# Kernel optimization log

Hardware: AMD Instinct MI355X
Metric: run time of the kernel (lower is better)

Reference implementation:

```python
import jax, jax.numpy as jnp
import numpy as np

N, E = 50000, 800000
IN_DIM, OUT_DIM, REL_DIM = 128, 64, 32
NEG_SLOPE = 0.01  # torch F.leaky_relu default


def setup_inputs() -> dict:
    key = jax.random.key(0)
    ks = jax.random.split(key, 12)
    return {
        "h": jax.random.normal(ks[0], (N, IN_DIM), jnp.float32),
        "relation": jax.random.normal(ks[1], (E, REL_DIM), jnp.float32),
        "score": jax.random.normal(ks[2], (E, 1), jnp.float32),
        "timestamp": jax.random.normal(ks[3], (E, 1), jnp.float32),
        "src": jax.random.randint(ks[4], (E,), 0, N, jnp.int32),
        "dst": jax.random.randint(ks[5], (E,), 0, N, jnp.int32),
        "W_n": jax.random.normal(ks[6], (IN_DIM, OUT_DIM), jnp.float32) / np.sqrt(IN_DIM),
        "W_r": jax.random.normal(ks[7], (REL_DIM, OUT_DIM), jnp.float32) / np.sqrt(REL_DIM),
        "W_s": jax.random.normal(ks[8], (1, OUT_DIM), jnp.float32),
        "W_t": jax.random.normal(ks[9], (1, OUT_DIM), jnp.float32),
        "a": jax.random.normal(ks[10], (5 * OUT_DIM,), jnp.float32) / np.sqrt(5 * OUT_DIM),
    }


def reference(h, relation, score, timestamp, src, dst, W_n, W_r, W_s, W_t, a):
    D = W_n.shape[1]
    z = h @ W_n                     # (N, D)
    er = relation @ W_r             # (E, D)
    es = score @ W_s                # (E, D)
    et = timestamp @ W_t            # (E, D)
    z_src = z[src]                  # (E, D) gather
    z_dst = z[dst]                  # (E, D) gather
    # attn_fc on concat([z_src, z_dst, er, es, et]) == sum of slice dot-products
    a1, a2, a3, a4, a5 = (a[0:D], a[D:2*D], a[2*D:3*D], a[3*D:4*D], a[4*D:5*D])
    logit = z_src @ a1 + z_dst @ a2 + er @ a3 + es @ a4 + et @ a5  # (E,)
    logit = jnp.where(logit >= 0, logit, NEG_SLOPE * logit)        # leaky_relu
    # segment softmax over edges grouped by dst node
    n = z.shape[0]
    seg_max = jax.ops.segment_max(logit, dst, num_segments=n)     # (N,)
    ex = jnp.exp(logit - seg_max[dst])                             # (E,)
    seg_sum = jax.ops.segment_sum(ex, dst, num_segments=n)        # (N,)
    alpha = ex / seg_sum[dst]                                      # (E,)
    # weighted scatter-sum of source features to dst nodes
    h_out = jax.ops.segment_sum(alpha[:, None] * z_src, dst, num_segments=n)  # (N, D)
    return h_out
```

## Files before the change

### kernel.cpp

```cpp
#include <hip/hip_runtime.h>

#define IN_DIM 128
#define OUT_DIM 64
#define REL_DIM 32
#define NEG_SLOPE 0.01f
#define CAP 64
#define EPB 1024
#define BCAP 1536
#define HSTRIDE 800

__global__ __launch_bounds__(256) void k_node(const float* __restrict__ h,
                                              const float* __restrict__ W_n,
                                              const float* __restrict__ a,
                                              float* __restrict__ z,
                                              float* __restrict__ s1,
                                              float* __restrict__ s2, int n) {
    __shared__ float hs[IN_DIM * 65];
    __shared__ float s1p[4][64], s2p[4][64];
    int base = blockIdx.x * 64;

    for (int i = threadIdx.x; i < 64 * 32; i += 256) {
        int r = i >> 5;
        int c4 = i & 31;
        float4 v = make_float4(0.f, 0.f, 0.f, 0.f);
        if (base + r < n) v = ((const float4*)(h + (size_t)(base + r) * IN_DIM))[c4];
        int k0 = c4 * 4;
        hs[(k0 + 0) * 65 + r] = v.x;
        hs[(k0 + 1) * 65 + r] = v.y;
        hs[(k0 + 2) * 65 + r] = v.z;
        hs[(k0 + 3) * 65 + r] = v.w;
    }
    __syncthreads();

    int lane = threadIdx.x & 63;
    int w = __builtin_amdgcn_readfirstlane(threadIdx.x >> 6);
    int c0 = w * 16;
    int row = base + lane;

    float acc[16];
    #pragma unroll
    for (int j = 0; j < 16; ++j) acc[j] = 0.f;

    const float* __restrict__ Wslice = W_n + c0;
    #pragma unroll 4
    for (int k = 0; k < IN_DIM; ++k) {
        float hv = hs[k * 65 + lane];
        const float* __restrict__ Wr = Wslice + k * OUT_DIM;
        #pragma unroll
        for (int j = 0; j < 16; ++j) acc[j] = fmaf(hv, Wr[j], acc[j]);
    }

    float p1 = 0.f, p2 = 0.f;
    #pragma unroll
    for (int j = 0; j < 16; ++j) {
        p1 = fmaf(acc[j], a[c0 + j], p1);
        p2 = fmaf(acc[j], a[OUT_DIM + c0 + j], p2);
    }
    s1p[w][lane] = p1;
    s2p[w][lane] = p2;

    if (row < n) {
        float4* zp = (float4*)(z + (size_t)row * OUT_DIM + c0);
        zp[0] = make_float4(acc[0], acc[1], acc[2], acc[3]);
        zp[1] = make_float4(acc[4], acc[5], acc[6], acc[7]);
        zp[2] = make_float4(acc[8], acc[9], acc[10], acc[11]);
        zp[3] = make_float4(acc[12], acc[13], acc[14], acc[15]);
    }
    __syncthreads();
    if (threadIdx.x < 64 && base + (int)threadIdx.x < n) {
        int l = threadIdx.x;
        s1[base + l] = s1p[0][l] + s1p[1][l] + s1p[2][l] + s1p[3][l];
        s2[base + l] = s2p[0][l] + s2p[1][l] + s2p[2][l] + s2p[3][l];
    }
}

__global__ __launch_bounds__(256) void k_hist(const int* __restrict__ dst,
                                              int* __restrict__ hist, int E, int nbkt) {
    __shared__ int lh[HSTRIDE];
    int t = threadIdx.x;
    for (int i = t; i < nbkt; i += 256) lh[i] = 0;
    __syncthreads();
    int e0 = blockIdx.x * EPB;
    #pragma unroll
    for (int i = 0; i < EPB / 256; ++i) {
        int e = e0 + i * 256 + t;
        if (e < E) atomicAdd(&lh[dst[e] >> 6], 1);
    }
    __syncthreads();
    for (int b = t; b < nbkt; b += 256)
        hist[(size_t)blockIdx.x * HSTRIDE + b] = lh[b];
}

__global__ __launch_bounds__(1024) void k_scan(int* __restrict__ hist,
                                               int* __restrict__ bcnt, int nblk) {
    __shared__ int tmp[1024];
    int b = blockIdx.x;
    int t = threadIdx.x;
    int v = (t < nblk) ? hist[(size_t)t * HSTRIDE + b] : 0;
    tmp[t] = v;
    __syncthreads();
    #pragma unroll
    for (int o = 1; o < 1024; o <<= 1) {
        int x = (t >= o) ? tmp[t - o] : 0;
        __syncthreads();
        tmp[t] += x;
        __syncthreads();
    }
    if (t < nblk) hist[(size_t)t * HSTRIDE + b] = tmp[t] - v;
    if (t == 0) bcnt[b] = tmp[1023];
}

__global__ __launch_bounds__(256) void k_scatter(const float* __restrict__ rel,
                                                 const float* __restrict__ score,
                                                 const float* __restrict__ ts,
                                                 const int* __restrict__ src,
                                                 const int* __restrict__ dst,
                                                 const float* __restrict__ s1,
                                                 const float* __restrict__ s2,
                                                 const float* __restrict__ W_r,
                                                 const float* __restrict__ W_s,
                                                 const float* __restrict__ W_t,
                                                 const float* __restrict__ a,
                                                 const int* __restrict__ hist,
                                                 int2* __restrict__ rec2,
                                                 int E, int nbkt) {
    __shared__ __align__(16) float cw[36];
    __shared__ int   lsrc[EPB], ldst[EPB];
    __shared__ float lsc[EPB],  lts[EPB];
    __shared__ int   lrank[HSTRIDE], lbase[HSTRIDE];
    int t = threadIdx.x;
    int e0 = blockIdx.x * EPB;

    if (t < REL_DIM) {
        const float* a3 = a + 2 * OUT_DIM;
        float acc = 0.f;
        #pragma unroll
        for (int d2 = 0; d2 < OUT_DIM; ++d2)
            acc = fmaf(W_r[t * OUT_DIM + d2], a3[d2], acc);
        cw[t] = acc;
    } else if (t == 32) {
        float acc = 0.f;
        for (int d2 = 0; d2 < OUT_DIM; ++d2) acc = fmaf(W_s[d2], a[3 * OUT_DIM + d2], acc);
        cw[32] = acc;
    } else if (t == 33) {
        float acc = 0.f;
        for (int d2 = 0; d2 < OUT_DIM; ++d2) acc = fmaf(W_t[d2], a[4 * OUT_DIM + d2], acc);
        cw[33] = acc;
    }
    for (int i = t; i < nbkt; i += 256) {
        lrank[i] = 0;
        lbase[i] = hist[(size_t)blockIdx.x * HSTRIDE + i];
    }
    #pragma unroll
    for (int i = 0; i < EPB / 256; ++i) {
        int le = i * 256 + t;
        int e = e0 + le;
        if (e < E) {
            lsrc[le] = src[e];
            ldst[le] = dst[e];
            lsc[le]  = score[e];
            lts[le]  = ts[e];
        }
    }
    __syncthreads();

    int g = t >> 3;
    int sub = t & 7;
    #pragma unroll 1
    for (int it = 0; it < EPB / 32; ++it) {
        int le = it * 32 + g;
        int e = e0 + le;
        if (e < E) {
            float4 w4 = ((const float4*)cw)[sub];
            float4 v = ((const float4*)rel)[(size_t)e * 8 + sub];
            float dot = v.x * w4.x + v.y * w4.y + v.z * w4.z + v.w * w4.w;
            dot += __shfl_xor(dot, 1, 8);
            dot += __shfl_xor(dot, 2, 8);
            dot += __shfl_xor(dot, 4, 8);
            if (sub == 0) {
                int s = lsrc[le], d = ldst[le];
                float lg = dot + s1[s] + s2[d] + lsc[le] * cw[32] + lts[le] * cw[33];
                lg = (lg >= 0.f) ? lg : NEG_SLOPE * lg;
                int b = d >> 6;
                int lr = atomicAdd(&lrank[b], 1);
                int pos = lbase[b] + lr;
                if (pos < BCAP)
                    rec2[(size_t)b * BCAP + pos] =
                        make_int2((int)(((unsigned)d << 16) | (unsigned)s),
                                  __float_as_int(lg));
            }
        }
    }
}

__global__ __launch_bounds__(512) void k_out2(const int* __restrict__ bcnt,
                                              const int2* __restrict__ rec2,
                                              const float* __restrict__ z,
                                              float* __restrict__ out, int n) {
    __shared__ int2 seg[64][CAP];
    __shared__ int scnt[64];
    int b = blockIdx.x;
    int tid = threadIdx.x;
    if (tid < 64) scnt[tid] = 0;
    __syncthreads();

    int cnt = bcnt[b];
    if (cnt > BCAP) cnt = BCAP;
    const int2* rb = rec2 + (size_t)b * BCAP;
    for (int i = tid; i < cnt; i += 512) {
        int2 r = rb[i];
        int dl = (int)((((unsigned)r.x) >> 16) & 63u);
        int rk = atomicAdd(&scnt[dl], 1);
        if (rk < CAP) seg[dl][rk] = make_int2(r.x & 0xffff, r.y);
    }
    __syncthreads();

    int lane = tid & 63;
    int w = tid >> 6;
    int eg = lane >> 4;
    int dl4 = lane & 15;
    for (int k = 0; k < 8; ++k) {
        int dl = w * 8 + k;
        int node = b * 64 + dl;
        if (node >= n) break;
        int deg = min(scnt[dl], CAP);
        float4 acc = make_float4(0.f, 0.f, 0.f, 0.f);
        if (deg > 0) {
            int2 pe = make_int2(0, (int)0xff800000u);
            if (lane < deg) pe = seg[dl][lane];
            float v = __int_as_float(pe.y);
            float m = v;
            #pragma unroll
            for (int o = 32; o > 0; o >>= 1) m = fmaxf(m, __shfl_xor(m, o, 64));
            float ex = __expf(v - m);
            float ssum = ex;
            #pragma unroll
            for (int o = 32; o > 0; o >>= 1) ssum += __shfl_xor(ssum, o, 64);
            float alpha = ex * (1.0f / ssum);
            for (int j0 = 0; j0 < deg; j0 += 4) {
                int j = j0 + eg;
                int jc = (j < 64) ? j : 63;
                float wj = __shfl(alpha, jc, 64);
                int sj = __shfl(pe.x, jc, 64);
                if (j < deg) {
                    float4 zv = ((const float4*)(z + (size_t)sj * OUT_DIM))[dl4];
                    acc.x = fmaf(wj, zv.x, acc.x);
                    acc.y = fmaf(wj, zv.y, acc.y);
                    acc.z = fmaf(wj, zv.z, acc.z);
                    acc.w = fmaf(wj, zv.w, acc.w);
                }
            }
        }
        #pragma unroll
        for (int o = 16; o <= 32; o <<= 1) {
            acc.x += __shfl_xor(acc.x, o, 64);
            acc.y += __shfl_xor(acc.y, o, 64);
            acc.z += __shfl_xor(acc.z, o, 64);
            acc.w += __shfl_xor(acc.w, o, 64);
        }
        if (eg == 0) ((float4*)(out + (size_t)node * OUT_DIM))[dl4] = acc;
    }
}

extern "C" void kernel_launch(void* const* d_in, const int* in_sizes, int n_in,
                              void* d_out, int out_size, void* d_ws, size_t ws_size,
                              hipStream_t stream) {
    const float* h         = (const float*)d_in[0];
    const float* relation  = (const float*)d_in[1];
    const float* score     = (const float*)d_in[2];
    const float* timestamp = (const float*)d_in[3];
    const int*   src       = (const int*)d_in[4];
    const int*   dst       = (const int*)d_in[5];
    const float* W_n       = (const float*)d_in[6];
    const float* W_r       = (const float*)d_in[7];
    const float* W_s       = (const float*)d_in[8];
    const float* W_t       = (const float*)d_in[9];
    const float* a         = (const float*)d_in[10];

    int n = in_sizes[0] / IN_DIM;
    int E = in_sizes[4];
    int nbkt = (n + 63) >> 6;
    int nblk = (E + EPB - 1) / EPB;

    float* ws   = (float*)d_ws;
    float* z    = ws;
    float* s1   = z + (size_t)n * OUT_DIM;
    float* s2   = s1 + n;
    int*   bcnt = (int*)(s2 + n);
    int*   hist = bcnt + HSTRIDE;
    int2*  rec2 = (int2*)(hist + (size_t)nblk * HSTRIDE);

    float* out = (float*)d_out;

    k_node<<<(n + 63) / 64, 256, 0, stream>>>(h, W_n, a, z, s1, s2, n);
    k_hist<<<nblk, 256, 0, stream>>>(dst, hist, E, nbkt);
    k_scan<<<nbkt, 1024, 0, stream>>>(hist, bcnt, nblk);
    k_scatter<<<nblk, 256, 0, stream>>>(relation, score, timestamp, src, dst,
                                        s1, s2, W_r, W_s, W_t, a, hist, rec2, E, nbkt);
    k_out2<<<nbkt, 512, 0, stream>>>(bcnt, rec2, z, out, n);
}
```

Measured before the change: 295.8 us.

## Fuse dst histogram into node GEMM kernel and widen scatter blocks to 1024 threads

The separate histogram kernel is folded into k_node, whose blocks grid-stride over the edge chunks before doing their node transform, which removes one launch. The scatter kernel now runs 1024 threads per block, each handling a quarter of the iterations, and reads src/dst/score/ts directly from global memory instead of staging them in LDS. This trades a launch and an LDS staging pass for extra syncs in k_node, more LDS use there (which may cut occupancy), and uncoalesced per-edge loads done only by the sub==0 lanes.

```diff
diff --git a/kernel.cpp b/kernel.cpp
--- a/kernel.cpp
+++ b/kernel.cpp
@@ -12,13 +12,32 @@
 __global__ __launch_bounds__(256) void k_node(const float* __restrict__ h,
                                               const float* __restrict__ W_n,
                                               const float* __restrict__ a,
+                                              const int* __restrict__ dst,
                                               float* __restrict__ z,
                                               float* __restrict__ s1,
-                                              float* __restrict__ s2, int n) {
+                                              float* __restrict__ s2,
+                                              int* __restrict__ hist,
+                                              int E, int nblk, int nbkt, int n) {
     __shared__ float hs[IN_DIM * 65];
     __shared__ float s1p[4][64], s2p[4][64];
+    __shared__ int lh[HSTRIDE];
+
+    for (int hb = blockIdx.x; hb < nblk; hb += gridDim.x) {
+        for (int i = threadIdx.x; i < nbkt; i += 256) lh[i] = 0;
+        __syncthreads();
+        int e0 = hb * EPB;
+        #pragma unroll
+        for (int i = 0; i < EPB / 256; ++i) {
+            int e = e0 + i * 256 + threadIdx.x;
+            if (e < E) atomicAdd(&lh[dst[e] >> 6], 1);
+        }
+        __syncthreads();
+        for (int b = threadIdx.x; b < nbkt; b += 256)
+            hist[(size_t)hb * HSTRIDE + b] = lh[b];
+        __syncthreads();
+    }
+
     int base = blockIdx.x * 64;
-
     for (int i = threadIdx.x; i < 64 * 32; i += 256) {
         int r = i >> 5;
         int c4 = i & 31;
@@ -74,23 +93,6 @@
     }
 }
 
-__global__ __launch_bounds__(256) void k_hist(const int* __restrict__ dst,
-                                              int* __restrict__ hist, int E, int nbkt) {
-    __shared__ int lh[HSTRIDE];
-    int t = threadIdx.x;
-    for (int i = t; i < nbkt; i += 256) lh[i] = 0;
-    __syncthreads();
-    int e0 = blockIdx.x * EPB;
-    #pragma unroll
-    for (int i = 0; i < EPB / 256; ++i) {
-        int e = e0 + i * 256 + t;
-        if (e < E) atomicAdd(&lh[dst[e] >> 6], 1);
-    }
-    __syncthreads();
-    for (int b = t; b < nbkt; b += 256)
-        hist[(size_t)blockIdx.x * HSTRIDE + b] = lh[b];
-}
-
 __global__ __launch_bounds__(1024) void k_scan(int* __restrict__ hist,
                                                int* __restrict__ bcnt, int nblk) {
     __shared__ int tmp[1024];
@@ -110,24 +112,22 @@
     if (t == 0) bcnt[b] = tmp[1023];
 }
 
-__global__ __launch_bounds__(256) void k_scatter(const float* __restrict__ rel,
-                                                 const float* __restrict__ score,
-                                                 const float* __restrict__ ts,
-                                                 const int* __restrict__ src,
-                                                 const int* __restrict__ dst,
-                                                 const float* __restrict__ s1,
-                                                 const float* __restrict__ s2,
-                                                 const float* __restrict__ W_r,
-                                                 const float* __restrict__ W_s,
-                                                 const float* __restrict__ W_t,
-                                                 const float* __restrict__ a,
-                                                 const int* __restrict__ hist,
-                                                 int2* __restrict__ rec2,
-                                                 int E, int nbkt) {
+__global__ __launch_bounds__(1024) void k_scatterF(const float* __restrict__ rel,
+                                                   const float* __restrict__ score,
+                                                   const float* __restrict__ ts,
+                                                   const int* __restrict__ src,
+                                                   const int* __restrict__ dst,
+                                                   const float* __restrict__ s1,
+                                                   const float* __restrict__ s2,
+                                                   const float* __restrict__ W_r,
+                                                   const float* __restrict__ W_s,
+                                                   const float* __restrict__ W_t,
+                                                   const float* __restrict__ a,
+                                                   const int* __restrict__ hist,
+                                                   int2* __restrict__ rec2,
+                                                   int E, int nbkt) {
     __shared__ __align__(16) float cw[36];
-    __shared__ int   lsrc[EPB], ldst[EPB];
-    __shared__ float lsc[EPB],  lts[EPB];
-    __shared__ int   lrank[HSTRIDE], lbase[HSTRIDE];
+    __shared__ int lrank[HSTRIDE], lbase[HSTRIDE];
     int t = threadIdx.x;
     int e0 = blockIdx.x * EPB;
 
@@ -147,28 +147,17 @@
         for (int d2 = 0; d2 < OUT_DIM; ++d2) acc = fmaf(W_t[d2], a[4 * OUT_DIM + d2], acc);
         cw[33] = acc;
     }
-    for (int i = t; i < nbkt; i += 256) {
+    for (int i = t; i < nbkt; i += 1024) {
         lrank[i] = 0;
         lbase[i] = hist[(size_t)blockIdx.x * HSTRIDE + i];
     }
-    #pragma unroll
-    for (int i = 0; i < EPB / 256; ++i) {
-        int le = i * 256 + t;
-        int e = e0 + le;
-        if (e < E) {
-            lsrc[le] = src[e];
-            ldst[le] = dst[e];
-            lsc[le]  = score[e];
-            lts[le]  = ts[e];
-        }
-    }
     __syncthreads();
 
     int g = t >> 3;
     int sub = t & 7;
-    #pragma unroll 1
-    for (int it = 0; it < EPB / 32; ++it) {
-        int le = it * 32 + g;
+    #pragma unroll 2
+    for (int it = 0; it < EPB / 128; ++it) {
+        int le = it * 128 + g;
         int e = e0 + le;
         if (e < E) {
             float4 w4 = ((const float4*)cw)[sub];
@@ -178,8 +167,8 @@
             dot += __shfl_xor(dot, 2, 8);
             dot += __shfl_xor(dot, 4, 8);
             if (sub == 0) {
-                int s = lsrc[le], d = ldst[le];
-                float lg = dot + s1[s] + s2[d] + lsc[le] * cw[32] + lts[le] * cw[33];
+                int s = src[e], d = dst[e];
+                float lg = dot + s1[s] + s2[d] + score[e] * cw[32] + ts[e] * cw[33];
                 lg = (lg >= 0.f) ? lg : NEG_SLOPE * lg;
                 int b = d >> 6;
                 int lr = atomicAdd(&lrank[b], 1);
@@ -292,10 +281,10 @@
 
     float* out = (float*)d_out;
 
-    k_node<<<(n + 63) / 64, 256, 0, stream>>>(h, W_n, a, z, s1, s2, n);
-    k_hist<<<nblk, 256, 0, stream>>>(dst, hist, E, nbkt);
+    k_node<<<(n + 63) / 64, 256, 0, stream>>>(h, W_n, a, dst, z, s1, s2,
+                                              hist, E, nblk, nbkt, n);
     k_scan<<<nbkt, 1024, 0, stream>>>(hist, bcnt, nblk);
-    k_scatter<<<nblk, 256, 0, stream>>>(relation, score, timestamp, src, dst,
-                                        s1, s2, W_r, W_s, W_t, a, hist, rec2, E, nbkt);
+    k_scatterF<<<nblk, 1024, 0, stream>>>(relation, score, timestamp, src, dst,
+                                          s1, s2, W_r, W_s, W_t, a, hist, rec2, E, nbkt);
     k_out2<<<nbkt, 512, 0, stream>>>(bcnt, rec2, z, out, n);
 }
```

New measurement: 292.2 us. No clear change (-1.2%).
